# Performance work log

Hardware: AMD Instinct MI355X
Metric: run time of the kernel (lower is better)

## Reference

```python
import jax, jax.numpy as jnp
import numpy as np

N = 16384      # nodes per NodeFlow layer
E = 262144     # edges per block (avg degree 16)
T = 327680     # total interpro indices (~20 per node)
P = 20000      # protein embedding table rows
INTERPRO = 30000
D_ESM = 1280
D = 1024
L = 5000       # labels_num
G = 2          # num_gcn


def setup_inputs() -> dict:
    key = jax.random.key(0)
    ks = jax.random.split(key, 16)
    protein_embedding = jax.random.normal(ks[0], (P, D_ESM), jnp.float32) * 0.02
    interpro_weight = jax.random.normal(ks[1], (INTERPRO, D), jnp.float32) * 0.02
    W_esm = jax.random.normal(ks[2], (D, D_ESM), jnp.float32) * (1.0 / np.sqrt(D_ESM))
    b_esm = jnp.zeros((D,), jnp.float32)
    bias1 = jnp.zeros((D,), jnp.float32)
    bias2 = jnp.zeros((D,), jnp.float32)
    w = jnp.ones((2,), jnp.float32)
    W_upd = jax.random.normal(ks[3], (G, D, 2 * D), jnp.float32) * (1.0 / np.sqrt(2 * D))
    b_upd = jnp.zeros((G, D), jnp.float32)
    W_out = jax.random.normal(ks[4], (L, D + D_ESM), jnp.float32) * (1.0 / np.sqrt(D + D_ESM))
    b_out = jnp.zeros((L,), jnp.float32)
    self_w = jax.random.uniform(ks[5], (E,), jnp.float32)
    ppi_w = jax.random.uniform(ks[6], (E,), jnp.float32)
    inputs = jax.random.randint(ks[7], (N,), 0, P)
    interpro_idx = jax.random.randint(ks[8], (T,), 0, INTERPRO)
    off = jnp.sort(jax.random.randint(ks[9], (N + 1,), 0, T))
    interpro_off = off.at[0].set(0).at[-1].set(T)  # include_last_offset convention
    src = jax.random.randint(ks[10], (E,), 0, N)
    dst = jax.random.randint(ks[11], (E,), 0, N)
    target_id = jax.random.randint(ks[12], (N,), 0, P)
    return dict(protein_embedding=protein_embedding, interpro_weight=interpro_weight,
                W_esm=W_esm, b_esm=b_esm, bias1=bias1, bias2=bias2, w=w,
                W_upd=W_upd, b_upd=b_upd, W_out=W_out, b_out=b_out,
                self_w=self_w, ppi_w=ppi_w, inputs=inputs,
                interpro_idx=interpro_idx, interpro_off=interpro_off,
                src=src, dst=dst, target_id=target_id)


def reference(protein_embedding, interpro_weight, W_esm, b_esm, bias1, bias2, w,
              W_upd, b_upd, W_out, b_out, self_w, ppi_w,
              inputs, interpro_idx, interpro_off, src, dst, target_id):
    # x1: ESM branch -> relu(Linear(esm[inputs]) + bias1)
    x1 = jax.nn.relu(protein_embedding[inputs] @ W_esm.T + b_esm + bias1)  # [N, D]
    # x2: EmbeddingBag(mode='sum', include_last_offset=True) + bias2
    seg = jnp.searchsorted(interpro_off, jnp.arange(T), side='right') - 1  # bag id per index
    bags = jax.ops.segment_sum(interpro_weight[interpro_idx], seg, num_segments=N)
    x2 = jax.nn.relu(bags + bias2)  # [N, D]
    # learned softmax mixture of the two branches
    sm = jax.nn.softmax(w)
    h = sm[0] * x1 + sm[1] * x2  # [N, D]
    # message passing layers: u_mul_e + sum for 'self' and 'ppi' edge weights,
    # then NodeUpdate: relu(Linear(cat(ppi_out, res))). Dropout is identity (eval).
    for i in range(G):
        msg = h[src]  # [E, D] irregular gather
        res = jax.ops.segment_sum(msg * self_w[:, None], dst, num_segments=N)
        ppi_out = jax.ops.segment_sum(msg * ppi_w[:, None], dst, num_segments=N)
        h = jax.nn.relu(jnp.concatenate([ppi_out, res], axis=1) @ W_upd[i].T + b_upd[i])
    last = jnp.concatenate([h, protein_embedding[target_id]], axis=1)  # [N, D+D_ESM]
    return last @ W_out.T + b_out  # [N, L]
```

## Files before the change

kernel.cpp:

```cpp
#include <hip/hip_runtime.h>

typedef unsigned short u16;
typedef u16 u16x4 __attribute__((ext_vector_type(4)));
typedef u16 u16x8 __attribute__((ext_vector_type(8)));
typedef float f32x4 __attribute__((ext_vector_type(4)));
typedef __bf16 bf16x8 __attribute__((ext_vector_type(8)));

#define NN 16384
#define EE 262144
#define DD 1024
#define DESM 1280
#define LL 5000
#define IPN 30000

static __device__ __forceinline__ u16 f2bf(float f) {
  unsigned u = __float_as_uint(f);
  u += 0x7FFF + ((u >> 16) & 1);
  return (u16)(u >> 16);
}
static __device__ __forceinline__ float bf2f(u16 h) {
  return __uint_as_float(((unsigned)h) << 16);
}

__global__ void cast_rows_k(const float* __restrict__ src, int scols,
                            const int* __restrict__ rowidx,
                            u16* __restrict__ dst, int dld, int dcol0,
                            int rows, int cols8 ) {
  long total = (long)rows * cols8;
  for (long i = blockIdx.x * (long)blockDim.x + threadIdx.x; i < total;
       i += (long)gridDim.x * blockDim.x) {
    int r = (int)(i / cols8);
    int k8 = (int)(i % cols8);
    int sr = rowidx ? rowidx[r] : r;
    const f32x4* s = (const f32x4*)(src + (size_t)sr * scols + (size_t)k8 * 8);
    f32x4 a = s[0], b = s[1];
    u16x8 o;
    o[0] = f2bf(a[0]); o[1] = f2bf(a[1]); o[2] = f2bf(a[2]); o[3] = f2bf(a[3]);
    o[4] = f2bf(b[0]); o[5] = f2bf(b[1]); o[6] = f2bf(b[2]); o[7] = f2bf(b[3]);
    *(u16x8*)(dst + (size_t)r * dld + dcol0 + (size_t)k8 * 8) = o;
  }
}

__global__ void embed_bag_k(const u16* __restrict__ W, const int* __restrict__ idx,
                            const int* __restrict__ off, const float* __restrict__ bias2,
                            float* __restrict__ x2pre) {
  int n = blockIdx.x;
  int t = threadIdx.x;
  int beg = off[n], end = off[n + 1];
  f32x4 acc = {0.f, 0.f, 0.f, 0.f};
  for (int p = beg; p < end; ++p) {
    int row = idx[p];
    u16x4 v = *(const u16x4*)(W + (size_t)row * DD + t * 4);
    acc[0] += bf2f(v[0]); acc[1] += bf2f(v[1]);
    acc[2] += bf2f(v[2]); acc[3] += bf2f(v[3]);
  }
  acc += *(const f32x4*)(bias2 + t * 4);
  *(f32x4*)(x2pre + (size_t)n * DD + t * 4) = acc;
}

__global__ void hist_k(const int* __restrict__ dst, int* __restrict__ counts) {
  int e = blockIdx.x * blockDim.x + threadIdx.x;
  if (e < EE) atomicAdd(&counts[dst[e]], 1);
}

__global__ void scan_k(const int* __restrict__ counts, int* __restrict__ row_off) {
  __shared__ int sh[256];
  int t = threadIdx.x;
  int s = 0;
  for (int i = 0; i < 64; ++i) s += counts[t * 64 + i];
  sh[t] = s;
  __syncthreads();
  if (t == 0) {
    int run = 0;
    for (int i = 0; i < 256; ++i) { int v = sh[i]; sh[i] = run; run += v; }
    row_off[NN] = run;
  }
  __syncthreads();
  int run = sh[t];
  for (int i = 0; i < 64; ++i) { row_off[t * 64 + i] = run; run += counts[t * 64 + i]; }
}

__global__ void scatter_k(const int* __restrict__ dst, int* __restrict__ cursor,
                          int* __restrict__ perm) {
  int e = blockIdx.x * blockDim.x + threadIdx.x;
  if (e < EE) {
    int pos = atomicAdd(&cursor[dst[e]], 1);
    perm[pos] = e;
  }
}

__global__ void aggregate_k(const u16* __restrict__ h, const int* __restrict__ row_off,
                            const int* __restrict__ perm, const float* __restrict__ self_w,
                            const float* __restrict__ ppi_w, const int* __restrict__ src,
                            u16* __restrict__ cat) {
  int n = blockIdx.x;
  int t = threadIdx.x;
  int beg = row_off[n], end = row_off[n + 1];
  f32x4 res = {0.f, 0.f, 0.f, 0.f}, ppi = {0.f, 0.f, 0.f, 0.f};
  for (int p = beg; p < end; ++p) {
    int e = perm[p];
    int s = src[e];
    float ws = self_w[e], wp = ppi_w[e];
    u16x4 m = *(const u16x4*)(h + (size_t)s * DD + t * 4);
    f32x4 mf = {bf2f(m[0]), bf2f(m[1]), bf2f(m[2]), bf2f(m[3])};
    res += ws * mf;
    ppi += wp * mf;
  }
  u16x4 o0, o1;
  o0[0] = f2bf(ppi[0]); o0[1] = f2bf(ppi[1]); o0[2] = f2bf(ppi[2]); o0[3] = f2bf(ppi[3]);
  o1[0] = f2bf(res[0]); o1[1] = f2bf(res[1]); o1[2] = f2bf(res[2]); o1[3] = f2bf(res[3]);
  *(u16x4*)(cat + (size_t)n * 2048 + t * 4) = o0;
  *(u16x4*)(cat + (size_t)n * 2048 + DD + t * 4) = o1;
}

static __device__ __forceinline__ void stage_half(const char* Gb, size_t ldb, int rowbase,
                                                  int rowmax, int kbyte, char* lds_half_w,
                                                  int s_rowoff, int s_inner) {
#pragma unroll
  for (int j = 0; j < 2; ++j) {
    int row = rowbase + j * 128 + s_rowoff;
    if (row > rowmax) row = rowmax;
    const char* src = Gb + (size_t)row * ldb + kbyte + s_inner;
    __builtin_amdgcn_global_load_lds(
        (const __attribute__((address_space(1))) void*)src,
        (__attribute__((address_space(3))) void*)(lds_half_w + j * 8192), 16, 0, 0);
  }
}

static __device__ __forceinline__ bf16x8 ldr(const char* kh, int row, int slot) {
  unsigned a = (unsigned)row * 64u +
               ((((unsigned)slot << 4) ^ ((((unsigned)row >> 1) & 3u) << 4)));
  return *(const bf16x8*)(kh + a);
}

template <int MODE>
__global__ __launch_bounds__(512, 2) void gemm8_k(
    const u16* __restrict__ A, const u16* __restrict__ B, int M, int N, int K,
    void* __restrict__ Cout, int ldc, const float* __restrict__ bias0,
    const float* __restrict__ bias1, const float* __restrict__ x2pre,
    const float* __restrict__ wmix) {
  __shared__ char lds[131072];
  char* ldsA = lds;
  char* ldsB = lds + 65536;
  const int tid = threadIdx.x;
  const int lane = tid & 63;
  const int wid = tid >> 6;
  const int wr = wid >> 2;
  const int wc = wid & 3;
  const int nwg = gridDim.x * gridDim.y;
  const int flat = blockIdx.x + gridDim.x * blockIdx.y;
  const int swz = (flat & 7) * (nwg >> 3) + (flat >> 3);
  const int row0 = (swz / gridDim.x) * 256;
  const int col0 = (swz % gridDim.x) * 256;
  const int NT = K >> 6;
  const size_t lda = (size_t)K * 2;
  const char* Ab = (const char*)A;
  const char* Bb = (const char*)B;
  const int l15 = lane & 15;
  const int slot = lane >> 4;
  const int s_rowoff = wid * 16 + (lane >> 2);
  const int s_inner = (((lane & 3) << 4) ^ (((lane >> 3) & 3) << 4));
  const int wb = wid * 1024;

  f32x4 acc[8][4];
#pragma unroll
  for (int m = 0; m < 8; ++m)
#pragma unroll
    for (int n = 0; n < 4; ++n) acc[m][n] = (f32x4){0.f, 0.f, 0.f, 0.f};

  const int k1 = (NT > 1) ? 128 : 0;
  stage_half(Bb, lda, col0, N - 1, 0,       ldsB + 0     + wb, s_rowoff, s_inner);
  stage_half(Ab, lda, row0, M - 1, 0,       ldsA + 0     + wb, s_rowoff, s_inner);
  stage_half(Ab, lda, row0, M - 1, 64,      ldsA + 16384 + wb, s_rowoff, s_inner);
  stage_half(Bb, lda, col0, N - 1, 64,      ldsB + 16384 + wb, s_rowoff, s_inner);
  stage_half(Bb, lda, col0, N - 1, k1,      ldsB + 32768 + wb, s_rowoff, s_inner);
  stage_half(Ab, lda, row0, M - 1, k1,      ldsA + 32768 + wb, s_rowoff, s_inner);
  stage_half(Bb, lda, col0, N - 1, k1 + 64, ldsB + 49152 + wb, s_rowoff, s_inner);
  asm volatile("s_waitcnt vmcnt(6)" ::: "memory");
  __builtin_amdgcn_s_barrier();

  bf16x8 afP[4], afQ[4], bqP[4], bqQ[4];
#pragma unroll
  for (int m = 0; m < 4; ++m) afP[m] = ldr(ldsA, wr * 128 + m * 16 + l15, slot);
#pragma unroll
  for (int n = 0; n < 4; ++n) bqP[n] = ldr(ldsB, wc * 64 + n * 16 + l15, slot);

  for (int t = 0; t < NT; ++t) {
    const int d = t & 1;
    char* Ad = ldsA + d * 32768;
    char* Bd = ldsB + d * 32768;
    const char* Akh1 = Ad + 16384;
    const char* Bkh1 = Bd + 16384;
    const char* AkhN0 = ldsA + (d ^ 1) * 32768;
    const char* BkhN0 = ldsB + (d ^ 1) * 32768;
    const int ts1 = (t + 1 < NT) ? t + 1 : NT - 1;
    const int ts2 = (t + 2 < NT) ? t + 2 : NT - 1;

#pragma unroll
    for (int m = 0; m < 4; ++m) afQ[m] = ldr(Ad, wr * 128 + (m + 4) * 16 + l15, slot);
#pragma unroll
    for (int n = 0; n < 4; ++n) bqQ[n] = ldr(Bkh1, wc * 64 + n * 16 + l15, slot);
    stage_half(Ab, lda, row0, M - 1, ts1 * 128 + 64,
               ldsA + ((t + 1) & 1) * 32768 + 16384 + wb, s_rowoff, s_inner);
    __builtin_amdgcn_sched_barrier(0);
    __builtin_amdgcn_s_setprio(1);
#pragma unroll
    for (int m = 0; m < 4; ++m)
#pragma unroll
      for (int n = 0; n < 4; ++n)
        acc[m][n] = __builtin_amdgcn_mfma_f32_16x16x32_bf16(afP[m], bqP[n], acc[m][n], 0, 0, 0);
    __builtin_amdgcn_s_setprio(0);
    asm volatile("s_waitcnt vmcnt(8)" ::: "memory");
    __builtin_amdgcn_s_barrier();

#pragma unroll
    for (int m = 0; m < 4; ++m) afP[m] = ldr(Akh1, wr * 128 + (m + 4) * 16 + l15, slot);
    stage_half(Bb, lda, col0, N - 1, ts2 * 128, Bd + wb, s_rowoff, s_inner);
    __builtin_amdgcn_sched_barrier(0);
    __builtin_amdgcn_s_setprio(1);
#pragma unroll
    for (int m = 0; m < 4; ++m)
#pragma unroll
      for (int n = 0; n < 4; ++n)
        acc[m + 4][n] = __builtin_amdgcn_mfma_f32_16x16x32_bf16(afQ[m], bqP[n], acc[m + 4][n], 0, 0, 0);
    __builtin_amdgcn_s_setprio(0);
    __builtin_amdgcn_s_barrier();

#pragma unroll
    for (int m = 0; m < 4; ++m) afQ[m] = ldr(Akh1, wr * 128 + m * 16 + l15, slot);
    stage_half(Ab, lda, row0, M - 1, ts2 * 128, Ad + wb, s_rowoff, s_inner);
    __builtin_amdgcn_sched_barrier(0);
    __builtin_amdgcn_s_setprio(1);
#pragma unroll
    for (int m = 0; m < 4; ++m)
#pragma unroll
      for (int n = 0; n < 4; ++n)
        acc[m + 4][n] = __builtin_amdgcn_mfma_f32_16x16x32_bf16(afP[m], bqQ[n], acc[m + 4][n], 0, 0, 0);
    __builtin_amdgcn_s_setprio(0);
    asm volatile("s_waitcnt vmcnt(6)" ::: "memory");
    __builtin_amdgcn_s_barrier();

#pragma unroll
    for (int m = 0; m < 4; ++m) afP[m] = ldr(AkhN0, wr * 128 + m * 16 + l15, slot);
#pragma unroll
    for (int n = 0; n < 4; ++n) bqP[n] = ldr(BkhN0, wc * 64 + n * 16 + l15, slot);
    stage_half(Bb, lda, col0, N - 1, ts2 * 128 + 64, Bd + 16384 + wb, s_rowoff, s_inner);
    __builtin_amdgcn_sched_barrier(0);
    __builtin_amdgcn_s_setprio(1);
#pragma unroll
    for (int m = 0; m < 4; ++m)
#pragma unroll
      for (int n = 0; n < 4; ++n)
        acc[m][n] = __builtin_amdgcn_mfma_f32_16x16x32_bf16(afQ[m], bqQ[n], acc[m][n], 0, 0, 0);
    __builtin_amdgcn_s_setprio(0);
    __builtin_amdgcn_s_barrier();
  }

  float sm0 = 0.f, sm1 = 0.f;
  if (MODE == 0) {
    float w0 = wmix[0], w1 = wmix[1];
    float mx = fmaxf(w0, w1);
    float e0 = expf(w0 - mx), e1 = expf(w1 - mx);
    float inv = 1.f / (e0 + e1);
    sm0 = e0 * inv;
    sm1 = e1 * inv;
  }
  float bc[4];
  int cs[4];
#pragma unroll
  for (int n = 0; n < 4; ++n) {
    int c = col0 + wc * 64 + n * 16 + l15;
    cs[n] = c;
    bc[n] = (MODE == 2 && c >= N) ? 0.f : (bias0[c] + (MODE == 0 ? bias1[c] : 0.f));
  }
#pragma unroll
  for (int m = 0; m < 8; ++m) {
#pragma unroll
    for (int n = 0; n < 4; ++n) {
      int c = cs[n];
      if (MODE == 2 && c >= N) continue;
      int r0 = row0 + wr * 128 + m * 16 + slot * 4;
#pragma unroll
      for (int r = 0; r < 4; ++r) {
        float v = acc[m][n][r] + bc[n];
        int rr = r0 + r;
        if (MODE == 0) {
          float x1v = fmaxf(v, 0.f);
          float x2v = fmaxf(x2pre[(size_t)rr * DD + c], 0.f);
          ((u16*)Cout)[(size_t)rr * ldc + c] = f2bf(sm0 * x1v + sm1 * x2v);
        } else if (MODE == 1) {
          ((u16*)Cout)[(size_t)rr * ldc + c] = f2bf(fmaxf(v, 0.f));
        } else {
          ((float*)Cout)[(size_t)rr * ldc + c] = v;
        }
      }
    }
  }
}

extern "C" void kernel_launch(void* const* d_in, const int* in_sizes, int n_in,
                              void* d_out, int out_size, void* d_ws, size_t ws_size,
                              hipStream_t stream) {
  const float* esm   = (const float*)d_in[0];
  const float* ipw   = (const float*)d_in[1];
  const float* Wesm  = (const float*)d_in[2];
  const float* besm  = (const float*)d_in[3];
  const float* bias1 = (const float*)d_in[4];
  const float* bias2 = (const float*)d_in[5];
  const float* wmix  = (const float*)d_in[6];
  const float* Wupd  = (const float*)d_in[7];
  const float* bupd  = (const float*)d_in[8];
  const float* Wout  = (const float*)d_in[9];
  const float* bout  = (const float*)d_in[10];
  const float* selfw = (const float*)d_in[11];
  const float* ppiw  = (const float*)d_in[12];
  const int* inputs  = (const int*)d_in[13];
  const int* ipidx   = (const int*)d_in[14];
  const int* ipoff   = (const int*)d_in[15];
  const int* src     = (const int*)d_in[16];
  const int* dst     = (const int*)d_in[17];
  const int* tgt     = (const int*)d_in[18];
  float* out = (float*)d_out;

  char* ws = (char*)d_ws;
  size_t o = 0;
  auto take = [&](size_t b) {
    char* r = ws + o;
    o += (b + 255) & ~(size_t)255;
    return r;
  };
  u16* Wesm_b = (u16*)take(1024ull * 1280 * 2);
  u16* Wupd_b = (u16*)take(2ull * 1024 * 2048 * 2);
  u16* Wout_b = (u16*)take(5000ull * 2304 * 2);
  int* counts  = (int*)take((size_t)NN * 4);
  int* row_off = (int*)take((size_t)(NN + 1) * 4);
  int* cursor  = (int*)take((size_t)NN * 4);
  int* perm    = (int*)take((size_t)EE * 4);
  u16* h_b     = (u16*)take((size_t)NN * DD * 2);
  char* shared0 = ws + o;
  size_t x2_b = ((size_t)NN * DD * 4 + 255) & ~(size_t)255;
  size_t a1_b = ((size_t)NN * DESM * 2 + 255) & ~(size_t)255;
  float* x2pre = (float*)shared0;
  u16* A1     = (u16*)(shared0 + x2_b);
  u16* ipw_b  = (u16*)(shared0 + x2_b + a1_b);
  u16* cat_b  = (u16*)shared0;
  u16* A_last = (u16*)(shared0 + x2_b);

  cast_rows_k<<<2048, 256, 0, stream>>>(Wesm, 1280, nullptr, Wesm_b, 1280, 0, 1024, 160);
  cast_rows_k<<<2048, 256, 0, stream>>>(Wupd, 2048, nullptr, Wupd_b, 2048, 0, 2048, 256);
  cast_rows_k<<<2048, 256, 0, stream>>>(Wout, 2304, nullptr, Wout_b, 2304, 0, 5000, 288);
  cast_rows_k<<<4096, 256, 0, stream>>>(ipw, 1024, nullptr, ipw_b, 1024, 0, IPN, 128);

  embed_bag_k<<<NN, 256, 0, stream>>>(ipw_b, ipidx, ipoff, bias2, x2pre);

  cast_rows_k<<<4096, 256, 0, stream>>>(esm, 1280, inputs, A1, 1280, 0, NN, 160);

  hipMemsetAsync(counts, 0, (size_t)NN * 4, stream);
  hist_k<<<EE / 256, 256, 0, stream>>>(dst, counts);
  scan_k<<<1, 256, 0, stream>>>(counts, row_off);
  hipMemcpyAsync(cursor, row_off, (size_t)NN * 4, hipMemcpyDeviceToDevice, stream);
  scatter_k<<<EE / 256, 256, 0, stream>>>(dst, cursor, perm);

  gemm8_k<0><<<dim3(4, 64), 512, 0, stream>>>(A1, Wesm_b, NN, 1024, 1280, h_b, 1024,
                                              besm, bias1, x2pre, wmix);

  cast_rows_k<<<4096, 256, 0, stream>>>(esm, 1280, tgt, A_last, 2304, 1024, NN, 160);

  aggregate_k<<<NN, 256, 0, stream>>>(h_b, row_off, perm, selfw, ppiw, src, cat_b);
  gemm8_k<1><<<dim3(4, 64), 512, 0, stream>>>(cat_b, Wupd_b, NN, 1024, 2048, h_b, 1024,
                                              bupd, nullptr, nullptr, nullptr);

  aggregate_k<<<NN, 256, 0, stream>>>(h_b, row_off, perm, selfw, ppiw, src, cat_b);
  gemm8_k<1><<<dim3(4, 64), 512, 0, stream>>>(cat_b, Wupd_b + (size_t)1024 * 2048, NN, 1024,
                                              2048, A_last, 2304, bupd + 1024, nullptr,
                                              nullptr, nullptr);

  gemm8_k<2><<<dim3(20, 64), 512, 0, stream>>>(A_last, Wout_b, NN, 5000, 2304, out, 5000,
                                               bout, nullptr, nullptr, nullptr);
}
```

Measured before the change: 1.030 ms.

## Pack edge records, widen gather loads, and store bag sums in bf16

The scatter step now writes a packed (src, self_w, ppi_w) record per sorted edge, so aggregation skips the perm→src/weight indirection. The embedding-bag and aggregation kernels each handle two nodes per block with 8-wide bf16 loads and unrolled multi-row gathers to raise memory-level parallelism. The bag output is stored as bf16 with bias and relu applied, which halves that intermediate's traffic, and the buffer layout is adjusted so A_last no longer overlaps A1. The cost is some precision loss on x2 and a larger edge-record buffer.

```diff
diff --git a/kernel.cpp b/kernel.cpp
--- a/kernel.cpp
+++ b/kernel.cpp
@@ -43,19 +43,43 @@
 
 __global__ void embed_bag_k(const u16* __restrict__ W, const int* __restrict__ idx,
                             const int* __restrict__ off, const float* __restrict__ bias2,
-                            float* __restrict__ x2pre) {
-  int n = blockIdx.x;
-  int t = threadIdx.x;
-  int beg = off[n], end = off[n + 1];
-  f32x4 acc = {0.f, 0.f, 0.f, 0.f};
-  for (int p = beg; p < end; ++p) {
-    int row = idx[p];
-    u16x4 v = *(const u16x4*)(W + (size_t)row * DD + t * 4);
-    acc[0] += bf2f(v[0]); acc[1] += bf2f(v[1]);
-    acc[2] += bf2f(v[2]); acc[3] += bf2f(v[3]);
-  }
-  acc += *(const f32x4*)(bias2 + t * 4);
-  *(f32x4*)(x2pre + (size_t)n * DD + t * 4) = acc;
+                            u16* __restrict__ x2b) {
+  int node = blockIdx.x * 2 + (threadIdx.x >> 7);
+  int t = threadIdx.x & 127;
+  int beg = off[node], end = off[node + 1];
+  float a[8];
+#pragma unroll
+  for (int j = 0; j < 8; ++j) a[j] = 0.f;
+  int p = beg;
+  for (; p + 8 <= end; p += 8) {
+    u16x8 v[8];
+#pragma unroll
+    for (int q = 0; q < 8; ++q)
+      v[q] = *(const u16x8*)(W + (size_t)idx[p + q] * DD + t * 8);
+#pragma unroll
+    for (int q = 0; q < 8; ++q)
+#pragma unroll
+      for (int j = 0; j < 8; ++j) a[j] += bf2f(v[q][j]);
+  }
+  for (; p + 2 <= end; p += 2) {
+    u16x8 v0 = *(const u16x8*)(W + (size_t)idx[p] * DD + t * 8);
+    u16x8 v1 = *(const u16x8*)(W + (size_t)idx[p + 1] * DD + t * 8);
+#pragma unroll
+    for (int j = 0; j < 8; ++j) a[j] += bf2f(v0[j]) + bf2f(v1[j]);
+  }
+  if (p < end) {
+    u16x8 v0 = *(const u16x8*)(W + (size_t)idx[p] * DD + t * 8);
+#pragma unroll
+    for (int j = 0; j < 8; ++j) a[j] += bf2f(v0[j]);
+  }
+  f32x4 b0 = *(const f32x4*)(bias2 + t * 8);
+  f32x4 b1 = *(const f32x4*)(bias2 + t * 8 + 4);
+  u16x8 o;
+#pragma unroll
+  for (int j = 0; j < 4; ++j) o[j] = f2bf(fmaxf(a[j] + b0[j], 0.f));
+#pragma unroll
+  for (int j = 0; j < 4; ++j) o[j + 4] = f2bf(fmaxf(a[j + 4] + b1[j], 0.f));
+  *(u16x8*)(x2b + (size_t)node * DD + t * 8) = o;
 }
 
 __global__ void hist_k(const int* __restrict__ dst, int* __restrict__ counts) {
@@ -80,37 +104,65 @@
   for (int i = 0; i < 64; ++i) { row_off[t * 64 + i] = run; run += counts[t * 64 + i]; }
 }
 
-__global__ void scatter_k(const int* __restrict__ dst, int* __restrict__ cursor,
-                          int* __restrict__ perm) {
+__global__ void scatter_k(const int* __restrict__ dst, const int* __restrict__ src,
+                          const float* __restrict__ selfw, const float* __restrict__ ppiw,
+                          int* __restrict__ cursor, int4* __restrict__ rec) {
   int e = blockIdx.x * blockDim.x + threadIdx.x;
   if (e < EE) {
     int pos = atomicAdd(&cursor[dst[e]], 1);
-    perm[pos] = e;
+    int4 r;
+    r.x = src[e];
+    r.y = __float_as_int(selfw[e]);
+    r.z = __float_as_int(ppiw[e]);
+    r.w = 0;
+    rec[pos] = r;
   }
 }
 
 __global__ void aggregate_k(const u16* __restrict__ h, const int* __restrict__ row_off,
-                            const int* __restrict__ perm, const float* __restrict__ self_w,
-                            const float* __restrict__ ppi_w, const int* __restrict__ src,
-                            u16* __restrict__ cat) {
-  int n = blockIdx.x;
-  int t = threadIdx.x;
-  int beg = row_off[n], end = row_off[n + 1];
-  f32x4 res = {0.f, 0.f, 0.f, 0.f}, ppi = {0.f, 0.f, 0.f, 0.f};
-  for (int p = beg; p < end; ++p) {
-    int e = perm[p];
-    int s = src[e];
-    float ws = self_w[e], wp = ppi_w[e];
-    u16x4 m = *(const u16x4*)(h + (size_t)s * DD + t * 4);
-    f32x4 mf = {bf2f(m[0]), bf2f(m[1]), bf2f(m[2]), bf2f(m[3])};
-    res += ws * mf;
-    ppi += wp * mf;
-  }
-  u16x4 o0, o1;
-  o0[0] = f2bf(ppi[0]); o0[1] = f2bf(ppi[1]); o0[2] = f2bf(ppi[2]); o0[3] = f2bf(ppi[3]);
-  o1[0] = f2bf(res[0]); o1[1] = f2bf(res[1]); o1[2] = f2bf(res[2]); o1[3] = f2bf(res[3]);
-  *(u16x4*)(cat + (size_t)n * 2048 + t * 4) = o0;
-  *(u16x4*)(cat + (size_t)n * 2048 + DD + t * 4) = o1;
+                            const int4* __restrict__ rec, u16* __restrict__ cat) {
+  int node = blockIdx.x * 2 + (threadIdx.x >> 7);
+  int t = threadIdx.x & 127;
+  int beg = row_off[node], end = row_off[node + 1];
+  float res[8], ppi[8];
+#pragma unroll
+  for (int j = 0; j < 8; ++j) { res[j] = 0.f; ppi[j] = 0.f; }
+  int p = beg;
+  for (; p + 4 <= end; p += 4) {
+    int4 r[4];
+    u16x8 m[4];
+#pragma unroll
+    for (int q = 0; q < 4; ++q) r[q] = rec[p + q];
+#pragma unroll
+    for (int q = 0; q < 4; ++q)
+      m[q] = *(const u16x8*)(h + (size_t)r[q].x * DD + t * 8);
+#pragma unroll
+    for (int q = 0; q < 4; ++q) {
+      float ws = __int_as_float(r[q].y), wp = __int_as_float(r[q].z);
+#pragma unroll
+      for (int j = 0; j < 8; ++j) {
+        float f = bf2f(m[q][j]);
+        res[j] += ws * f;
+        ppi[j] += wp * f;
+      }
+    }
+  }
+  for (; p < end; ++p) {
+    int4 r0 = rec[p];
+    u16x8 m0 = *(const u16x8*)(h + (size_t)r0.x * DD + t * 8);
+    float ws = __int_as_float(r0.y), wp = __int_as_float(r0.z);
+#pragma unroll
+    for (int j = 0; j < 8; ++j) {
+      float f = bf2f(m0[j]);
+      res[j] += ws * f;
+      ppi[j] += wp * f;
+    }
+  }
+  u16x8 o0, o1;
+#pragma unroll
+  for (int j = 0; j < 8; ++j) { o0[j] = f2bf(ppi[j]); o1[j] = f2bf(res[j]); }
+  *(u16x8*)(cat + (size_t)node * 2048 + t * 8) = o0;
+  *(u16x8*)(cat + (size_t)node * 2048 + DD + t * 8) = o1;
 }
 
 static __device__ __forceinline__ void stage_half(const char* Gb, size_t ldb, int rowbase,
@@ -137,7 +189,7 @@
 __global__ __launch_bounds__(512, 2) void gemm8_k(
     const u16* __restrict__ A, const u16* __restrict__ B, int M, int N, int K,
     void* __restrict__ Cout, int ldc, const float* __restrict__ bias0,
-    const float* __restrict__ bias1, const float* __restrict__ x2pre,
+    const float* __restrict__ bias1, const u16* __restrict__ x2b,
     const float* __restrict__ wmix) {
   __shared__ char lds[131072];
   char* ldsA = lds;
@@ -286,7 +338,7 @@
         int rr = r0 + r;
         if (MODE == 0) {
           float x1v = fmaxf(v, 0.f);
-          float x2v = fmaxf(x2pre[(size_t)rr * DD + c], 0.f);
+          float x2v = bf2f(x2b[(size_t)rr * DD + c]);
           ((u16*)Cout)[(size_t)rr * ldc + c] = f2bf(sm0 * x1v + sm1 * x2v);
         } else if (MODE == 1) {
           ((u16*)Cout)[(size_t)rr * ldc + c] = f2bf(fmaxf(v, 0.f));
@@ -335,23 +387,23 @@
   int* counts  = (int*)take((size_t)NN * 4);
   int* row_off = (int*)take((size_t)(NN + 1) * 4);
   int* cursor  = (int*)take((size_t)NN * 4);
-  int* perm    = (int*)take((size_t)EE * 4);
+  int4* rec    = (int4*)take((size_t)EE * 16);
   u16* h_b     = (u16*)take((size_t)NN * DD * 2);
   char* shared0 = ws + o;
-  size_t x2_b = ((size_t)NN * DD * 4 + 255) & ~(size_t)255;
+  size_t x2_b = ((size_t)NN * DD * 2 + 255) & ~(size_t)255;
   size_t a1_b = ((size_t)NN * DESM * 2 + 255) & ~(size_t)255;
-  float* x2pre = (float*)shared0;
+  u16* x2b    = (u16*)shared0;
   u16* A1     = (u16*)(shared0 + x2_b);
   u16* ipw_b  = (u16*)(shared0 + x2_b + a1_b);
   u16* cat_b  = (u16*)shared0;
-  u16* A_last = (u16*)(shared0 + x2_b);
+  u16* A_last = (u16*)(shared0 + x2_b + a1_b);
 
   cast_rows_k<<<2048, 256, 0, stream>>>(Wesm, 1280, nullptr, Wesm_b, 1280, 0, 1024, 160);
   cast_rows_k<<<2048, 256, 0, stream>>>(Wupd, 2048, nullptr, Wupd_b, 2048, 0, 2048, 256);
   cast_rows_k<<<2048, 256, 0, stream>>>(Wout, 2304, nullptr, Wout_b, 2304, 0, 5000, 288);
   cast_rows_k<<<4096, 256, 0, stream>>>(ipw, 1024, nullptr, ipw_b, 1024, 0, IPN, 128);
 
-  embed_bag_k<<<NN, 256, 0, stream>>>(ipw_b, ipidx, ipoff, bias2, x2pre);
+  embed_bag_k<<<NN / 2, 256, 0, stream>>>(ipw_b, ipidx, ipoff, bias2, x2b);
 
   cast_rows_k<<<4096, 256, 0, stream>>>(esm, 1280, inputs, A1, 1280, 0, NN, 160);
 
@@ -359,18 +411,18 @@
   hist_k<<<EE / 256, 256, 0, stream>>>(dst, counts);
   scan_k<<<1, 256, 0, stream>>>(counts, row_off);
   hipMemcpyAsync(cursor, row_off, (size_t)NN * 4, hipMemcpyDeviceToDevice, stream);
-  scatter_k<<<EE / 256, 256, 0, stream>>>(dst, cursor, perm);
+  scatter_k<<<EE / 256, 256, 0, stream>>>(dst, src, selfw, ppiw, cursor, rec);
 
   gemm8_k<0><<<dim3(4, 64), 512, 0, stream>>>(A1, Wesm_b, NN, 1024, 1280, h_b, 1024,
-                                              besm, bias1, x2pre, wmix);
+                                              besm, bias1, x2b, wmix);
 
   cast_rows_k<<<4096, 256, 0, stream>>>(esm, 1280, tgt, A_last, 2304, 1024, NN, 160);
 
-  aggregate_k<<<NN, 256, 0, stream>>>(h_b, row_off, perm, selfw, ppiw, src, cat_b);
+  aggregate_k<<<NN / 2, 256, 0, stream>>>(h_b, row_off, rec, cat_b);
   gemm8_k<1><<<dim3(4, 64), 512, 0, stream>>>(cat_b, Wupd_b, NN, 1024, 2048, h_b, 1024,
                                               bupd, nullptr, nullptr, nullptr);
 
-  aggregate_k<<<NN, 256, 0, stream>>>(h_b, row_off, perm, selfw, ppiw, src, cat_b);
+  aggregate_k<<<NN / 2, 256, 0, stream>>>(h_b, row_off, rec, cat_b);
   gemm8_k<1><<<dim3(4, 64), 512, 0, stream>>>(cat_b, Wupd_b + (size_t)1024 * 2048, NN, 1024,
                                               2048, A_last, 2304, bupd + 1024, nullptr,
                                               nullptr, nullptr);
```

Result: faster. 930.4 us (-9.7%).
